# Kernel optimization log

Measured on AMD Instinct MI355X. Metric: run time of the kernel, lower is better.

Reference implementation:

```python
import jax, jax.numpy as jnp
import numpy as np

N = 100000   # nodes
E = 1600000  # edges
G = 1000     # graphs in batch
F = 16       # in_features
D = 128      # embed_dim
C = 100      # num_centroid
K = 2        # num_class
L = 3        # num_layers


def setup_inputs() -> dict:
    key = jax.random.key(0)
    ks = jax.random.split(key, 8)
    x = jax.random.normal(ks[0], (N, F), dtype=jnp.float32)
    edge_index = jax.random.randint(ks[1], (2, E), 0, N)
    batch = jnp.sort(jax.random.randint(ks[2], (N,), 0, G))
    # learned params (xavier-like scaled, per init code)
    W_embed = jax.random.normal(ks[3], (D, F), dtype=jnp.float32) * 0.1
    W_convs = jax.random.normal(ks[4], (L, D, D), dtype=jnp.float32) * 0.05
    centroids = jax.random.normal(ks[5], (C, D), dtype=jnp.float32) * 0.1
    W_out = jax.random.normal(ks[6], (K, C), dtype=jnp.float32) * 0.1
    b_out = jax.random.uniform(ks[7], (K,), jnp.float32, -1e-4, 1e-4)
    return {"x": x, "edge_index": edge_index, "batch": batch,
            "W_embed": W_embed, "W_convs": W_convs, "centroids": centroids,
            "W_out": W_out, "b_out": b_out}


def _gcn_conv(h, W, src, dst, deg_isqrt):
    # h: [N, D]; standard GCNConv with self-loops, no bias
    m = h @ W.T                                   # [N, D]
    coef = deg_isqrt[src] * deg_isqrt[dst]        # [E+N]
    msg = m[src] * coef[:, None]                  # gather + scale
    return jax.ops.segment_sum(msg, dst, num_segments=N)


def reference(x, edge_index, batch, W_embed, W_convs, centroids, W_out, b_out):
    src0, dst0 = edge_index[0], edge_index[1]
    loop = jnp.arange(N, dtype=src0.dtype)
    src = jnp.concatenate([src0, loop])           # A + I edges
    dst = jnp.concatenate([dst0, loop])
    deg = jax.ops.segment_sum(jnp.ones(src.shape[0], jnp.float32), dst, num_segments=N)
    deg_isqrt = jax.lax.rsqrt(jnp.maximum(deg, 1.0))

    h = x @ W_embed.T                             # embedding, no bias
    for i in range(L):
        h = _gcn_conv(h, W_convs[i], src, dst, deg_isqrt)
        h = jax.nn.relu(h)                        # manifold (Euclidean) nonlinearity

    # centroid Euclidean distances: [N, C] via ||a-b||^2 = |a|^2 + |b|^2 - 2ab
    x2 = jnp.sum(h * h, axis=1, keepdims=True)            # [N,1]
    c2 = jnp.sum(centroids * centroids, axis=1)[None, :]  # [1,C]
    d2 = jnp.maximum(x2 + c2 - 2.0 * (h @ centroids.T), 0.0)
    dist = jnp.sqrt(d2 + 1e-12)                            # [N,C]

    # mean-pool per graph
    sums = jax.ops.segment_sum(dist, batch, num_segments=G)           # [G,C]
    cnts = jax.ops.segment_sum(jnp.ones((N,), jnp.float32), batch, num_segments=G)
    pooled = sums / jnp.maximum(cnts, 1.0)[:, None]

    return pooled @ W_out.T + b_out               # [G, K]
```

## Files before the change

kernel.cpp:

```cpp
#include <hip/hip_runtime.h>
#include <hip/hip_bf16.h>
#include <hip/hip_fp16.h>

constexpr int N_ = 100000;
constexpr int E_ = 1600000;
constexpr int G_ = 1000;
constexpr int D_ = 128;
constexpr int C_ = 100;
constexpr int K_ = 2;
constexpr int L_ = 3;
constexpr int CAP_ = 64;
constexpr int NR_ = 8;
constexpr int RN_ = N_ / NR_;
constexpr int EPB_ = 1280;
constexpr int NCH_ = (E_ + EPB_ - 1) / EPB_;

using f16x8 = __attribute__((ext_vector_type(8))) _Float16;
using f16x4 = __attribute__((ext_vector_type(4))) _Float16;
using f32x4 = __attribute__((ext_vector_type(4))) float;

__global__ __launch_bounds__(256) void fill_pad_xcd(
    const int* __restrict__ srcv, const int* __restrict__ dstv,
    int* __restrict__ cur, int* __restrict__ csr) {
    int r = blockIdx.x & 7;
    int chunk = blockIdx.x >> 3;
    int lo = r * RN_;
    int hi = lo + RN_;
    int ebeg = chunk * EPB_;
    int eend = ebeg + EPB_; if (eend > E_) eend = E_;
    for (int e = ebeg + threadIdx.x; e < eend; e += 256) {
        int d = dstv[e];
        if (d >= lo && d < hi) {
            int pos = atomicAdd(&cur[d], 1);
            if (pos < CAP_) csr[(size_t)d * CAP_ + pos] = srcv[e];
        }
    }
}

__global__ void dis_kernel(const int* __restrict__ cur, float* __restrict__ dis) {
    int i = blockIdx.x * 256 + threadIdx.x;
    if (i < N_) dis[i] = 1.0f / sqrtf((float)(cur[i] + 1));
}

__global__ __launch_bounds__(128) void embed_kernel(
    const float* __restrict__ x, const float* __restrict__ Wemb,
    _Float16* __restrict__ h) {
    __shared__ float4 xs[64 * 4];
    int t = threadIdx.x;
    float w[16];
#pragma unroll
    for (int f = 0; f < 16; ++f) w[f] = Wemb[t * 16 + f];
    int n0 = blockIdx.x * 64;
    const float4* x4 = (const float4*)x;
    for (int idx = t; idx < 64 * 4; idx += 128) {
        int gi = n0 * 4 + idx;
        xs[idx] = (gi < N_ * 4) ? x4[gi] : make_float4(0.f, 0.f, 0.f, 0.f);
    }
    __syncthreads();
    int lim = min(64, N_ - n0);
    for (int j = 0; j < lim; ++j) {
        float4 x0 = xs[j * 4 + 0], x1 = xs[j * 4 + 1];
        float4 x2 = xs[j * 4 + 2], x3 = xs[j * 4 + 3];
        float acc = x0.x * w[0] + x0.y * w[1] + x0.z * w[2] + x0.w * w[3]
                  + x1.x * w[4] + x1.y * w[5] + x1.z * w[6] + x1.w * w[7]
                  + x2.x * w[8] + x2.y * w[9] + x2.z * w[10] + x2.w * w[11]
                  + x3.x * w[12] + x3.y * w[13] + x3.z * w[14] + x3.w * w[15];
        h[(size_t)(n0 + j) * 128 + t] = (_Float16)acc;
    }
}

template<int FP16OUT>
__global__ __launch_bounds__(256) void mfma_gemm(
    const _Float16* __restrict__ h, const float* __restrict__ W,
    void* __restrict__ outp, int ncols, const float* __restrict__ dis) {
    int t = threadIdx.x;
    int w = t >> 6;
    int l = t & 63;
    int l15 = l & 15;
    int g = l >> 4;
    int nb0 = blockIdx.x * 128;

    f16x8 afr[2][4];
#pragma unroll
    for (int cg = 0; cg < 2; ++cg) {
        int c = 16 * w + 64 * cg + l15;
#pragma unroll
        for (int ks = 0; ks < 4; ++ks) {
            f16x8 af = {0, 0, 0, 0, 0, 0, 0, 0};
            if (c < ncols) {
                const float* wp = &W[c * 128 + 32 * ks + 8 * g];
                float4 w0 = *(const float4*)wp;
                float4 w1 = *(const float4*)(wp + 4);
                af[0] = (_Float16)w0.x; af[1] = (_Float16)w0.y;
                af[2] = (_Float16)w0.z; af[3] = (_Float16)w0.w;
                af[4] = (_Float16)w1.x; af[5] = (_Float16)w1.y;
                af[6] = (_Float16)w1.z; af[7] = (_Float16)w1.w;
            }
            afr[cg][ks] = af;
        }
    }

    for (int nt = 0; nt < 8; ++nt) {
        int nb = nb0 + 16 * nt;
        int node = nb + l15;
        int nodeL = node < N_ ? node : 0;
        f16x8 bfr[4];
#pragma unroll
        for (int ks = 0; ks < 4; ++ks)
            bfr[ks] = *(const f16x8*)&h[(size_t)nodeL * 128 + 32 * ks + 8 * g];
        f32x4 acc0 = {0.f, 0.f, 0.f, 0.f};
        f32x4 acc1 = {0.f, 0.f, 0.f, 0.f};
#pragma unroll
        for (int ks = 0; ks < 4; ++ks) {
            acc0 = __builtin_amdgcn_mfma_f32_16x16x32_f16(afr[0][ks], bfr[ks], acc0, 0, 0, 0);
            acc1 = __builtin_amdgcn_mfma_f32_16x16x32_f16(afr[1][ks], bfr[ks], acc1, 0, 0, 0);
        }
        if (node < N_) {
            int cb = 16 * w + 4 * g;
            if (FP16OUT) {
                float s = dis[node];
                ushort* mh = (ushort*)outp;
                __half2 p01 = __float22half2_rn(make_float2(acc0[0] * s, acc0[1] * s));
                __half2 p23 = __float22half2_rn(make_float2(acc0[2] * s, acc0[3] * s));
                uint2 u0;
                u0.x = *(unsigned int*)&p01; u0.y = *(unsigned int*)&p23;
                *(uint2*)&mh[(size_t)node * 128 + cb] = u0;
                __half2 q01 = __float22half2_rn(make_float2(acc1[0] * s, acc1[1] * s));
                __half2 q23 = __float22half2_rn(make_float2(acc1[2] * s, acc1[3] * s));
                uint2 u1;
                u1.x = *(unsigned int*)&q01; u1.y = *(unsigned int*)&q23;
                *(uint2*)&mh[(size_t)node * 128 + cb + 64] = u1;
            } else {
                float* o = (float*)outp;
                *(float4*)&o[(size_t)node * 128 + cb] =
                    make_float4(acc0[0], acc0[1], acc0[2], acc0[3]);
                *(float4*)&o[(size_t)node * 128 + cb + 64] =
                    make_float4(acc1[0], acc1[1], acc1[2], acc1[3]);
            }
        }
    }
}

__device__ inline float4 h4f4(uint2 u) {
    float2 fa = __half22float2(*(__half2*)&u.x);
    float2 fb = __half22float2(*(__half2*)&u.y);
    return make_float4(fa.x, fa.y, fb.x, fb.y);
}

__global__ __launch_bounds__(256) void aggregate(
    const ushort* __restrict__ mh, _Float16* __restrict__ hout,
    const int* __restrict__ cur, const int* __restrict__ csr,
    const float* __restrict__ dis, float* __restrict__ x2out) {
    int t = threadIdx.x;
    int lane = t & 63;
    int l32 = lane & 31;
    int hbase = lane & 32;
    int node = blockIdx.x * 8 + ((t >> 6) << 1) + (hbase >> 5);
    const uint2* m2 = (const uint2*)mh;

    float4 acc0 = h4f4(m2[(size_t)node * 32 + l32]);
    float4 acc1 = make_float4(0.f, 0.f, 0.f, 0.f);
    int deg = cur[node]; if (deg > CAP_) deg = CAP_;
    int beg = node * CAP_, end = beg + deg;
    for (int base = beg; base < end; base += 32) {
        int cnt = end - base; if (cnt > 32) cnt = 32;
        int myidx = (l32 < cnt) ? csr[base + l32] : 0;
        int j = 0;
        for (; j + 8 <= cnt; j += 8) {
            int s0 = __shfl(myidx, hbase + j);
            int s1 = __shfl(myidx, hbase + j + 1);
            int s2 = __shfl(myidx, hbase + j + 2);
            int s3 = __shfl(myidx, hbase + j + 3);
            int s4 = __shfl(myidx, hbase + j + 4);
            int s5 = __shfl(myidx, hbase + j + 5);
            int s6 = __shfl(myidx, hbase + j + 6);
            int s7 = __shfl(myidx, hbase + j + 7);
            uint2 u0 = m2[(size_t)s0 * 32 + l32];
            uint2 u1 = m2[(size_t)s1 * 32 + l32];
            uint2 u2 = m2[(size_t)s2 * 32 + l32];
            uint2 u3 = m2[(size_t)s3 * 32 + l32];
            uint2 u4 = m2[(size_t)s4 * 32 + l32];
            uint2 u5 = m2[(size_t)s5 * 32 + l32];
            uint2 u6 = m2[(size_t)s6 * 32 + l32];
            uint2 u7 = m2[(size_t)s7 * 32 + l32];
            float4 v0 = h4f4(u0), v1 = h4f4(u1), v2 = h4f4(u2), v3 = h4f4(u3);
            float4 v4 = h4f4(u4), v5 = h4f4(u5), v6 = h4f4(u6), v7 = h4f4(u7);
            acc0.x += (v0.x + v1.x) + (v2.x + v3.x);
            acc0.y += (v0.y + v1.y) + (v2.y + v3.y);
            acc0.z += (v0.z + v1.z) + (v2.z + v3.z);
            acc0.w += (v0.w + v1.w) + (v2.w + v3.w);
            acc1.x += (v4.x + v5.x) + (v6.x + v7.x);
            acc1.y += (v4.y + v5.y) + (v6.y + v7.y);
            acc1.z += (v4.z + v5.z) + (v6.z + v7.z);
            acc1.w += (v4.w + v5.w) + (v6.w + v7.w);
        }
        for (; j + 4 <= cnt; j += 4) {
            int s0 = __shfl(myidx, hbase + j);
            int s1 = __shfl(myidx, hbase + j + 1);
            int s2 = __shfl(myidx, hbase + j + 2);
            int s3 = __shfl(myidx, hbase + j + 3);
            uint2 u0 = m2[(size_t)s0 * 32 + l32];
            uint2 u1 = m2[(size_t)s1 * 32 + l32];
            uint2 u2 = m2[(size_t)s2 * 32 + l32];
            uint2 u3 = m2[(size_t)s3 * 32 + l32];
            float4 v0 = h4f4(u0), v1 = h4f4(u1), v2 = h4f4(u2), v3 = h4f4(u3);
            acc0.x += (v0.x + v1.x) + (v2.x + v3.x);
            acc0.y += (v0.y + v1.y) + (v2.y + v3.y);
            acc0.z += (v0.z + v1.z) + (v2.z + v3.z);
            acc0.w += (v0.w + v1.w) + (v2.w + v3.w);
        }
        for (; j < cnt; ++j) {
            int s = __shfl(myidx, hbase + j);
            float4 v = h4f4(m2[(size_t)s * 32 + l32]);
            acc1.x += v.x; acc1.y += v.y; acc1.z += v.z; acc1.w += v.w;
        }
    }
    float di = dis[node];
    f16x4 hq;
    hq[0] = (_Float16)fmaxf(di * (acc0.x + acc1.x), 0.f);
    hq[1] = (_Float16)fmaxf(di * (acc0.y + acc1.y), 0.f);
    hq[2] = (_Float16)fmaxf(di * (acc0.z + acc1.z), 0.f);
    hq[3] = (_Float16)fmaxf(di * (acc0.w + acc1.w), 0.f);
    *(f16x4*)&hout[(size_t)node * 128 + (l32 << 2)] = hq;
    if (x2out) {
        float h0 = (float)hq[0], h1 = (float)hq[1];
        float h2 = (float)hq[2], h3 = (float)hq[3];
        float p = h0 * h0 + h1 * h1 + h2 * h2 + h3 * h3;
        p += __shfl_xor(p, 1);
        p += __shfl_xor(p, 2);
        p += __shfl_xor(p, 4);
        p += __shfl_xor(p, 8);
        p += __shfl_xor(p, 16);
        if (l32 == 0) x2out[node] = p;
    }
}

__global__ __launch_bounds__(128) void pool_final(
    const float* __restrict__ dots, const float* __restrict__ x2,
    const float* __restrict__ cent, const int* __restrict__ batch,
    const float* __restrict__ W_out, const float* __restrict__ b_out,
    float* __restrict__ out) {
    __shared__ float sp[128];
    int g = blockIdx.x;
    int t = threadIdx.x;
    int lo = 0, hi = N_;
    while (lo < hi) { int mid = (lo + hi) >> 1; if (batch[mid] < g) lo = mid + 1; else hi = mid; }
    int s = lo;
    hi = N_;
    while (lo < hi) { int mid = (lo + hi) >> 1; if (batch[mid] < g + 1) lo = mid + 1; else hi = mid; }
    int e = lo;
    float pooledv = 0.f;
    if (t < C_) {
        float cv = 0.f;
#pragma unroll 4
        for (int k = 0; k < 128; ++k) {
            float v = (float)(_Float16)cent[t * 128 + k];
            cv += v * v;
        }
        float a0 = 0.f, a1 = 0.f, a2 = 0.f, a3 = 0.f;
        int n = s;
        for (; n + 4 <= e; n += 4) {
            float d0 = dots[(size_t)(n    ) * 128 + t];
            float d1 = dots[(size_t)(n + 1) * 128 + t];
            float d2 = dots[(size_t)(n + 2) * 128 + t];
            float d3 = dots[(size_t)(n + 3) * 128 + t];
            float x0 = x2[n], x1 = x2[n + 1], x2v = x2[n + 2], x3 = x2[n + 3];
            a0 += sqrtf(fmaxf(x0  + cv - 2.f * d0, 0.f) + 1e-12f);
            a1 += sqrtf(fmaxf(x1  + cv - 2.f * d1, 0.f) + 1e-12f);
            a2 += sqrtf(fmaxf(x2v + cv - 2.f * d2, 0.f) + 1e-12f);
            a3 += sqrtf(fmaxf(x3  + cv - 2.f * d3, 0.f) + 1e-12f);
        }
        for (; n < e; ++n) {
            float d = dots[(size_t)n * 128 + t];
            a0 += sqrtf(fmaxf(x2[n] + cv - 2.f * d, 0.f) + 1e-12f);
        }
        float inv = 1.0f / fmaxf((float)(e - s), 1.0f);
        pooledv = (a0 + a1 + a2 + a3) * inv;
    }
    sp[t] = pooledv;
    __syncthreads();
    if (t < K_) {
        float acc = 0.f;
        for (int c = 0; c < C_; ++c) acc += sp[c] * W_out[t * C_ + c];
        out[g * K_ + t] = acc + b_out[t];
    }
}

extern "C" void kernel_launch(void* const* d_in, const int* in_sizes, int n_in,
                              void* d_out, int out_size, void* d_ws, size_t ws_size,
                              hipStream_t stream) {
    const float* x       = (const float*)d_in[0];
    const int*   eidx    = (const int*)d_in[1];
    const int*   batch   = (const int*)d_in[2];
    const float* W_embed = (const float*)d_in[3];
    const float* W_convs = (const float*)d_in[4];
    const float* cent    = (const float*)d_in[5];
    const float* W_out   = (const float*)d_in[6];
    const float* b_out   = (const float*)d_in[7];
    float* out = (float*)d_out;

    char* p = (char*)d_ws;
    _Float16* h  = (_Float16*)p; p += (size_t)N_ * D_ * 2;
    float*  dots = (float*)p;  p += (size_t)N_ * D_ * 4;
    ushort* mh   = (ushort*)p; p += (size_t)N_ * D_ * 2;
    int*   cur  = (int*)p;   p += (size_t)N_ * 4;
    float* dis  = (float*)p; p += (size_t)N_ * 4;
    int*   csr  = (int*)p;   p += (size_t)N_ * CAP_ * 4;
    float* x2   = (float*)p; p += (size_t)N_ * 4;

    const int* esrc = eidx;
    const int* edst = eidx + E_;

    hipMemsetAsync(cur, 0, (size_t)N_ * 4, stream);

    fill_pad_xcd<<<NR_ * NCH_, 256, 0, stream>>>(esrc, edst, cur, csr);
    dis_kernel<<<(N_ + 255) / 256, 256, 0, stream>>>(cur, dis);

    embed_kernel<<<(N_ + 63) / 64, 128, 0, stream>>>(x, W_embed, h);

    int ngb = (N_ + 127) / 128;
    for (int l = 0; l < L_; ++l) {
        mfma_gemm<1><<<ngb, 256, 0, stream>>>(h, W_convs + (size_t)l * D_ * D_,
                                              (void*)mh, 128, dis);
        aggregate<<<N_ / 8, 256, 0, stream>>>(mh, h, cur, csr, dis,
                                              (l == L_ - 1) ? x2 : nullptr);
    }

    mfma_gemm<0><<<ngb, 256, 0, stream>>>(h, cent, (void*)dots, 100, nullptr);
    pool_final<<<G_, 128, 0, stream>>>(dots, x2, cent, batch, W_out, b_out, out);
}
```

Baseline: 405.4 us.

## Fuse centroid distance and mean-pool into the final MFMA GEMM epilogue

The centroid dot-product GEMM now computes the distances directly in its epilogue and accumulates per-graph sums in shared memory with atomics, spilling to global atomics when a graph falls outside the block's local window. This removes the N×128 fp32 dots buffer write and re-read, and the per-graph pooling kernel that walked it. A tiny final kernel applies the mean and the output linear layer. The trade-off is LDS and global atomic contention, plus float atomics that make the summation order nondeterministic.

```diff
diff --git a/kernel.cpp b/kernel.cpp
--- a/kernel.cpp
+++ b/kernel.cpp
@@ -14,6 +14,7 @@
 constexpr int RN_ = N_ / NR_;
 constexpr int EPB_ = 1280;
 constexpr int NCH_ = (E_ + EPB_ - 1) / EPB_;
+constexpr int NGMAX_ = 8;
 
 using f16x8 = __attribute__((ext_vector_type(8))) _Float16;
 using f16x4 = __attribute__((ext_vector_type(4))) _Float16;
@@ -69,10 +70,9 @@
     }
 }
 
-template<int FP16OUT>
 __global__ __launch_bounds__(256) void mfma_gemm(
     const _Float16* __restrict__ h, const float* __restrict__ W,
-    void* __restrict__ outp, int ncols, const float* __restrict__ dis) {
+    ushort* __restrict__ mh, const float* __restrict__ dis) {
     int t = threadIdx.x;
     int w = t >> 6;
     int l = t & 63;
@@ -86,9 +86,89 @@
         int c = 16 * w + 64 * cg + l15;
 #pragma unroll
         for (int ks = 0; ks < 4; ++ks) {
+            const float* wp = &W[c * 128 + 32 * ks + 8 * g];
+            float4 w0 = *(const float4*)wp;
+            float4 w1 = *(const float4*)(wp + 4);
+            f16x8 af;
+            af[0] = (_Float16)w0.x; af[1] = (_Float16)w0.y;
+            af[2] = (_Float16)w0.z; af[3] = (_Float16)w0.w;
+            af[4] = (_Float16)w1.x; af[5] = (_Float16)w1.y;
+            af[6] = (_Float16)w1.z; af[7] = (_Float16)w1.w;
+            afr[cg][ks] = af;
+        }
+    }
+
+    for (int nt = 0; nt < 8; ++nt) {
+        int nb = nb0 + 16 * nt;
+        int node = nb + l15;
+        int nodeL = node < N_ ? node : 0;
+        f16x8 bfr[4];
+#pragma unroll
+        for (int ks = 0; ks < 4; ++ks)
+            bfr[ks] = *(const f16x8*)&h[(size_t)nodeL * 128 + 32 * ks + 8 * g];
+        f32x4 acc0 = {0.f, 0.f, 0.f, 0.f};
+        f32x4 acc1 = {0.f, 0.f, 0.f, 0.f};
+#pragma unroll
+        for (int ks = 0; ks < 4; ++ks) {
+            acc0 = __builtin_amdgcn_mfma_f32_16x16x32_f16(afr[0][ks], bfr[ks], acc0, 0, 0, 0);
+            acc1 = __builtin_amdgcn_mfma_f32_16x16x32_f16(afr[1][ks], bfr[ks], acc1, 0, 0, 0);
+        }
+        if (node < N_) {
+            int cb = 16 * w + 4 * g;
+            float s = dis[node];
+            __half2 p01 = __float22half2_rn(make_float2(acc0[0] * s, acc0[1] * s));
+            __half2 p23 = __float22half2_rn(make_float2(acc0[2] * s, acc0[3] * s));
+            uint2 u0;
+            u0.x = *(unsigned int*)&p01; u0.y = *(unsigned int*)&p23;
+            *(uint2*)&mh[(size_t)node * 128 + cb] = u0;
+            __half2 q01 = __float22half2_rn(make_float2(acc1[0] * s, acc1[1] * s));
+            __half2 q23 = __float22half2_rn(make_float2(acc1[2] * s, acc1[3] * s));
+            uint2 u1;
+            u1.x = *(unsigned int*)&q01; u1.y = *(unsigned int*)&q23;
+            *(uint2*)&mh[(size_t)node * 128 + cb + 64] = u1;
+        }
+    }
+}
+
+__global__ __launch_bounds__(256) void mfma_dist_pool(
+    const _Float16* __restrict__ h, const float* __restrict__ cent,
+    const float* __restrict__ x2, const int* __restrict__ batch,
+    float* __restrict__ pooled) {
+    __shared__ float c2s[128];
+    __shared__ float pl[NGMAX_][C_];
+    int t = threadIdx.x;
+    int w = t >> 6;
+    int l = t & 63;
+    int l15 = l & 15;
+    int g = l >> 4;
+    int nb0 = blockIdx.x * 128;
+
+    if (t < 128) {
+        float cv = 0.f;
+        if (t < C_) {
+#pragma unroll 4
+            for (int k = 0; k < 128; ++k) {
+                float v = (float)(_Float16)cent[t * 128 + k];
+                cv += v * v;
+            }
+        }
+        c2s[t] = cv;
+    }
+    for (int idx = t; idx < NGMAX_ * C_; idx += 256)
+        ((float*)pl)[idx] = 0.f;
+    __syncthreads();
+
+    int g_base = batch[nb0 < N_ ? nb0 : N_ - 1];
+
+    f16x8 afr[2][4];
+#pragma unroll
+    for (int cg = 0; cg < 2; ++cg) {
+        int c = 16 * w + 64 * cg + l15;
+#pragma unroll
+        for (int ks = 0; ks < 4; ++ks) {
             f16x8 af = {0, 0, 0, 0, 0, 0, 0, 0};
-            if (c < ncols) {
-                const float* wp = &W[c * 128 + 32 * ks + 8 * g];
+            if (c < C_) {
+                const float* wp = &cent[c * 128 + 32 * ks + 8 * g];
                 float4 w0 = *(const float4*)wp;
                 float4 w1 = *(const float4*)(wp + 4);
                 af[0] = (_Float16)w0.x; af[1] = (_Float16)w0.y;
@@ -116,27 +196,48 @@
             acc1 = __builtin_amdgcn_mfma_f32_16x16x32_f16(afr[1][ks], bfr[ks], acc1, 0, 0, 0);
         }
         if (node < N_) {
+            float xv = x2[node];
+            int gb = batch[node];
+            int gl = gb - g_base;
             int cb = 16 * w + 4 * g;
-            if (FP16OUT) {
-                float s = dis[node];
-                ushort* mh = (ushort*)outp;
-                __half2 p01 = __float22half2_rn(make_float2(acc0[0] * s, acc0[1] * s));
-                __half2 p23 = __float22half2_rn(make_float2(acc0[2] * s, acc0[3] * s));
-                uint2 u0;
-                u0.x = *(unsigned int*)&p01; u0.y = *(unsigned int*)&p23;
-                *(uint2*)&mh[(size_t)node * 128 + cb] = u0;
-                __half2 q01 = __float22half2_rn(make_float2(acc1[0] * s, acc1[1] * s));
-                __half2 q23 = __float22half2_rn(make_float2(acc1[2] * s, acc1[3] * s));
-                uint2 u1;
-                u1.x = *(unsigned int*)&q01; u1.y = *(unsigned int*)&q23;
-                *(uint2*)&mh[(size_t)node * 128 + cb + 64] = u1;
+            if (gl >= 0 && gl < NGMAX_) {
+#pragma unroll
+                for (int j = 0; j < 4; ++j) {
+                    float d = sqrtf(fmaxf(xv + c2s[cb + j] - 2.0f * acc0[j], 0.f) + 1e-12f);
+                    atomicAdd(&pl[gl][cb + j], d);
+                }
+                int c1 = cb + 64;
+                if (c1 < C_) {
+#pragma unroll
+                    for (int j = 0; j < 4; ++j) {
+                        float d = sqrtf(fmaxf(xv + c2s[c1 + j] - 2.0f * acc1[j], 0.f) + 1e-12f);
+                        atomicAdd(&pl[gl][c1 + j], d);
+                    }
+                }
             } else {
-                float* o = (float*)outp;
-                *(float4*)&o[(size_t)node * 128 + cb] =
-                    make_float4(acc0[0], acc0[1], acc0[2], acc0[3]);
-                *(float4*)&o[(size_t)node * 128 + cb + 64] =
-                    make_float4(acc1[0], acc1[1], acc1[2], acc1[3]);
+#pragma unroll
+                for (int j = 0; j < 4; ++j) {
+                    float d = sqrtf(fmaxf(xv + c2s[cb + j] - 2.0f * acc0[j], 0.f) + 1e-12f);
+                    atomicAdd(&pooled[(size_t)gb * C_ + cb + j], d);
+                }
+                int c1 = cb + 64;
+                if (c1 < C_) {
+#pragma unroll
+                    for (int j = 0; j < 4; ++j) {
+                        float d = sqrtf(fmaxf(xv + c2s[c1 + j] - 2.0f * acc1[j], 0.f) + 1e-12f);
+                        atomicAdd(&pooled[(size_t)gb * C_ + c1 + j], d);
+                    }
+                }
             }
+        }
+    }
+    __syncthreads();
+    for (int idx = t; idx < NGMAX_ * C_; idx += 256) {
+        float v = ((float*)pl)[idx];
+        if (v != 0.f) {
+            int gl = idx / C_, c = idx - gl * C_;
+            int gg = g_base + gl;
+            if (gg < G_) atomicAdd(&pooled[(size_t)gg * C_ + c], v);
         }
     }
 }
@@ -235,55 +336,23 @@
     }
 }
 
-__global__ __launch_bounds__(128) void pool_final(
-    const float* __restrict__ dots, const float* __restrict__ x2,
-    const float* __restrict__ cent, const int* __restrict__ batch,
-    const float* __restrict__ W_out, const float* __restrict__ b_out,
-    float* __restrict__ out) {
-    __shared__ float sp[128];
-    int g = blockIdx.x;
-    int t = threadIdx.x;
+__global__ void final_out(const float* __restrict__ pooled,
+                          const int* __restrict__ batch,
+                          const float* __restrict__ W_out, const float* __restrict__ b_out,
+                          float* __restrict__ out) {
+    int i = blockIdx.x * 256 + threadIdx.x;
+    if (i >= G_ * K_) return;
+    int g = i >> 1, k = i & 1;
     int lo = 0, hi = N_;
     while (lo < hi) { int mid = (lo + hi) >> 1; if (batch[mid] < g) lo = mid + 1; else hi = mid; }
     int s = lo;
     hi = N_;
     while (lo < hi) { int mid = (lo + hi) >> 1; if (batch[mid] < g + 1) lo = mid + 1; else hi = mid; }
     int e = lo;
-    float pooledv = 0.f;
-    if (t < C_) {
-        float cv = 0.f;
-#pragma unroll 4
-        for (int k = 0; k < 128; ++k) {
-            float v = (float)(_Float16)cent[t * 128 + k];
-            cv += v * v;
-        }
-        float a0 = 0.f, a1 = 0.f, a2 = 0.f, a3 = 0.f;
-        int n = s;
-        for (; n + 4 <= e; n += 4) {
-            float d0 = dots[(size_t)(n    ) * 128 + t];
-            float d1 = dots[(size_t)(n + 1) * 128 + t];
-            float d2 = dots[(size_t)(n + 2) * 128 + t];
-            float d3 = dots[(size_t)(n + 3) * 128 + t];
-            float x0 = x2[n], x1 = x2[n + 1], x2v = x2[n + 2], x3 = x2[n + 3];
-            a0 += sqrtf(fmaxf(x0  + cv - 2.f * d0, 0.f) + 1e-12f);
-            a1 += sqrtf(fmaxf(x1  + cv - 2.f * d1, 0.f) + 1e-12f);
-            a2 += sqrtf(fmaxf(x2v + cv - 2.f * d2, 0.f) + 1e-12f);
-            a3 += sqrtf(fmaxf(x3  + cv - 2.f * d3, 0.f) + 1e-12f);
-        }
-        for (; n < e; ++n) {
-            float d = dots[(size_t)n * 128 + t];
-            a0 += sqrtf(fmaxf(x2[n] + cv - 2.f * d, 0.f) + 1e-12f);
-        }
-        float inv = 1.0f / fmaxf((float)(e - s), 1.0f);
-        pooledv = (a0 + a1 + a2 + a3) * inv;
-    }
-    sp[t] = pooledv;
-    __syncthreads();
-    if (t < K_) {
-        float acc = 0.f;
-        for (int c = 0; c < C_; ++c) acc += sp[c] * W_out[t * C_ + c];
-        out[g * K_ + t] = acc + b_out[t];
-    }
+    float inv = 1.0f / fmaxf((float)(e - s), 1.0f);
+    float acc = 0.f;
+    for (int c = 0; c < C_; ++c) acc += pooled[g * C_ + c] * W_out[k * C_ + c];
+    out[i] = acc * inv + b_out[k];
 }
 
 extern "C" void kernel_launch(void* const* d_in, const int* in_sizes, int n_in,
@@ -301,17 +370,18 @@
 
     char* p = (char*)d_ws;
     _Float16* h  = (_Float16*)p; p += (size_t)N_ * D_ * 2;
-    float*  dots = (float*)p;  p += (size_t)N_ * D_ * 4;
     ushort* mh   = (ushort*)p; p += (size_t)N_ * D_ * 2;
     int*   cur  = (int*)p;   p += (size_t)N_ * 4;
     float* dis  = (float*)p; p += (size_t)N_ * 4;
     int*   csr  = (int*)p;   p += (size_t)N_ * CAP_ * 4;
     float* x2   = (float*)p; p += (size_t)N_ * 4;
+    float* pool = (float*)p; p += (size_t)G_ * C_ * 4;
 
     const int* esrc = eidx;
     const int* edst = eidx + E_;
 
     hipMemsetAsync(cur, 0, (size_t)N_ * 4, stream);
+    hipMemsetAsync(pool, 0, (size_t)G_ * C_ * 4, stream);
 
     fill_pad_xcd<<<NR_ * NCH_, 256, 0, stream>>>(esrc, edst, cur, csr);
     dis_kernel<<<(N_ + 255) / 256, 256, 0, stream>>>(cur, dis);
@@ -320,12 +390,11 @@
 
     int ngb = (N_ + 127) / 128;
     for (int l = 0; l < L_; ++l) {
-        mfma_gemm<1><<<ngb, 256, 0, stream>>>(h, W_convs + (size_t)l * D_ * D_,
-                                              (void*)mh, 128, dis);
+        mfma_gemm<<<ngb, 256, 0, stream>>>(h, W_convs + (size_t)l * D_ * D_, mh, dis);
         aggregate<<<N_ / 8, 256, 0, stream>>>(mh, h, cur, csr, dis,
                                               (l == L_ - 1) ? x2 : nullptr);
     }
 
-    mfma_gemm<0><<<ngb, 256, 0, stream>>>(h, cent, (void*)dots, 100, nullptr);
-    pool_final<<<G_, 128, 0, stream>>>(dots, x2, cent, batch, W_out, b_out, out);
-}
+    mfma_dist_pool<<<ngb, 256, 0, stream>>>(h, cent, x2, batch, pool);
+    final_out<<<(G_ * K_ + 255) / 256, 256, 0, stream>>>(pool, batch, W_out, b_out, out);
+}
```

Result: slower. 464.6 us (+14.6%).
